# Optimization experiments

Hardware: AMD Instinct MI355X
Metric: run time of the kernel (lower is better)

The kernel has to match this reference:

```python
import jax, jax.numpy as jnp
import numpy as np

B, T, D, H = 2, 2048, 1024, 16
DH = D // H  # 64


def setup_inputs() -> dict:
    key = jax.random.key(0)
    ks = jax.random.split(key, 8)
    s = 0.02
    return {
        "x": jax.random.normal(ks[0], (B, T, D), jnp.float32),
        "mask": jnp.tril(jnp.ones((T, T), dtype=bool)),  # causal self-attention mask
        "wq": jax.random.normal(ks[1], (H, DH, D), jnp.float32) * s,
        "wk": jax.random.normal(ks[2], (H, DH, D), jnp.float32) * s,
        "wv": jax.random.normal(ks[3], (H, DH, D), jnp.float32) * s,
        "w1": jax.random.normal(ks[4], (4 * D, D), jnp.float32) * s,
        "b1": jnp.zeros((4 * D,), jnp.float32),
        "w2": jax.random.normal(ks[5], (D, 4 * D), jnp.float32) * s,
        "b2": jnp.zeros((D,), jnp.float32),
    }


def reference(x, mask, wq, wk, wv, w1, b1, w2, b2):
    # Per-head projections (MultiHeadLinear, bias=False, stacked on axis=-3):
    # q/k/v: [B, H, T, DH]
    q = jnp.einsum('btd,hed->bhte', x, wq)
    k = jnp.einsum('btd,hed->bhte', x, wk)
    v = jnp.einsum('btd,hed->bhte', x, wv)
    # logits = q @ k^T scaled by 1/sqrt(d_head): [B, H, T, T]
    logits = jnp.einsum('bhte,bhse->bhts', q, k) * (DH ** -0.5)
    logits = jnp.where(mask, logits, -jnp.inf)
    attn = jax.nn.softmax(logits, axis=-1)
    attn_out = jnp.einsum('bhts,bhse->bhte', attn, v)  # [B, H, T, DH]
    attn_out = jnp.transpose(attn_out, (0, 2, 1, 3)).reshape(B, T, D)
    # Note: output is x + ffw(x + attn_out) per the original forward.
    h = x + attn_out
    ffn = jax.nn.gelu(h @ w1.T + b1, approximate=False) @ w2.T + b2
    return x + ffn
```

## Files before the change

kernel.cpp:

```cpp
#include <hip/hip_runtime.h>
#include <hip/hip_bf16.h>
#include <cmath>

typedef __bf16 bf16;
typedef __bf16 bf16x8 __attribute__((ext_vector_type(8)));
typedef __bf16 bf16x4 __attribute__((ext_vector_type(4)));
typedef __bf16 bf16x2 __attribute__((ext_vector_type(2)));
typedef float  f32x4  __attribute__((ext_vector_type(4)));
typedef float  f32x16 __attribute__((ext_vector_type(16)));
typedef int    i32x4  __attribute__((ext_vector_type(4)));

#define B_   2
#define T_   2048
#define D_   1024
#define H_   16
#define DH_  64
#define BT_  (B_ * T_)
#define DFF_ (4 * D_)

#define GLDS(gp, lp) __builtin_amdgcn_global_load_lds( \
    (const __attribute__((address_space(1))) void*)(gp), \
    (__attribute__((address_space(3))) void*)(lp), 16, 0, 0)
#define VMCNT(n) asm volatile("s_waitcnt vmcnt(" #n ")" ::: "memory")

__global__ void cvt_f32_bf16(const float* __restrict__ src, bf16* __restrict__ dst, int n) {
    int i = (blockIdx.x * blockDim.x + threadIdx.x) * 4;
    if (i >= n) return;
    float4 v = *(const float4*)(src + i);
    bf16x4 o;
    o[0] = (bf16)v.x; o[1] = (bf16)v.y; o[2] = (bf16)v.z; o[3] = (bf16)v.w;
    *(bf16x4*)(dst + i) = o;
}

__device__ __forceinline__ float gelu_f(float v) {
    return 0.5f * v * (1.0f + erff(v * 0.70710678118654752f));
}

__device__ __forceinline__ int pkbf(float a, float b) {
    bf16x2 v; v[0] = (bf16)a; v[1] = (bf16)b;
    return __builtin_bit_cast(int, v);
}

__global__ __launch_bounds__(256) void transpose_v(
    const bf16* __restrict__ vrow, bf16* __restrict__ vt)
{
    __shared__ bf16 tile[64][72];
    const int tb = blockIdx.x;
    const int eb = blockIdx.y;
    const int b  = blockIdx.z;
    const int c  = threadIdx.x;

    const bf16* src = vrow + ((long)b * T_ + tb * 64) * 1024 + eb * 64;
    #pragma unroll
    for (int j = 0; j < 2; j++) {
        int ch = c + j * 256;
        int r = ch >> 3, s = ch & 7;
        *(bf16x8*)&tile[r][s * 8] = *(const bf16x8*)&src[(long)r * 1024 + s * 8];
    }
    __syncthreads();
    bf16* dst = vt + ((long)b * 1024 + eb * 64) * 2048 + tb * 64;
    #pragma unroll
    for (int j = 0; j < 2; j++) {
        int ch = c + j * 256;
        int r = ch >> 3, s = ch & 7;
        bf16x8 o;
        #pragma unroll
        for (int k = 0; k < 8; k++) o[k] = tile[s * 8 + k][r];
        *(bf16x8*)&dst[(long)r * 2048 + s * 8] = o;
    }
}

template <int EPI>
__global__ __launch_bounds__(256) void gemm_bt(
    const bf16* __restrict__ A, const bf16* __restrict__ Bt,
    void* __restrict__ outp, void* __restrict__ outp2, const float* __restrict__ bias,
    const float* __restrict__ resid, int M, int N, int K)
{
    __shared__ __align__(16) bf16 As[2][128 * 32];
    __shared__ __align__(16) bf16 Bs[2][128 * 32];
    const int tid  = threadIdx.x;
    const int lane = tid & 63;
    const int w    = tid >> 6;
    const int wr   = w >> 1, wc = w & 1;
    const int g    = lane >> 4, cc = lane & 15;
    const int m0   = blockIdx.y * 128, n0 = blockIdx.x * 128;
    const int NT   = K >> 5;

    f32x4 acc[4][4] = {};

    const int c0 = tid, c1 = tid + 256;
    const bf16* gA0 = A  + (long)(m0 + (c0 >> 2)) * K + ((c0 & 3) << 3);
    const bf16* gA1 = A  + (long)(m0 + (c1 >> 2)) * K + ((c1 & 3) << 3);
    const bf16* gB0 = Bt + (long)(n0 + (c0 >> 2)) * K + ((c0 & 3) << 3);
    const bf16* gB1 = Bt + (long)(n0 + (c1 >> 2)) * K + ((c1 & 3) << 3);

    auto stage = [&](int t) {
        const int buf = t & 1;
        const long k0 = (long)t << 5;
        GLDS(gA0 + k0, &As[buf][c0 * 8]);
        GLDS(gA1 + k0, &As[buf][c1 * 8]);
        GLDS(gB0 + k0, &Bs[buf][c0 * 8]);
        GLDS(gB1 + k0, &Bs[buf][c1 * 8]);
    };

    stage(0);
    VMCNT(0);
    __builtin_amdgcn_s_barrier();

    for (int t = 0; t < NT; ++t) {
        const bf16* Ab = As[t & 1];
        const bf16* Bb = Bs[t & 1];
        if (t + 1 < NT) stage(t + 1);

        bf16x8 af[4], bfr[4];
        #pragma unroll
        for (int mi = 0; mi < 4; mi++)
            af[mi] = *(const bf16x8*)&Ab[(wr * 64 + mi * 16 + cc) * 32 + g * 8];
        #pragma unroll
        for (int ni = 0; ni < 4; ni++)
            bfr[ni] = *(const bf16x8*)&Bb[(wc * 64 + ni * 16 + cc) * 32 + g * 8];
        #pragma unroll
        for (int mi = 0; mi < 4; mi++)
            #pragma unroll
            for (int ni = 0; ni < 4; ni++)
                acc[mi][ni] = __builtin_amdgcn_mfma_f32_16x16x32_bf16(af[mi], bfr[ni], acc[mi][ni], 0, 0, 0);

        VMCNT(0);
        __builtin_amdgcn_s_barrier();
    }

    #pragma unroll
    for (int mi = 0; mi < 4; mi++) {
        #pragma unroll
        for (int ni = 0; ni < 4; ni++) {
            #pragma unroll
            for (int r = 0; r < 4; r++) {
                int grow = m0 + wr * 64 + mi * 16 + g * 4 + r;
                int gcol = n0 + wc * 64 + ni * 16 + cc;
                float v = acc[mi][ni][r];
                if constexpr (EPI == 3) {
                    if (gcol < 2048)
                        ((bf16*)outp)[(long)grow * 2048 + gcol] = (bf16)v;
                    else
                        ((bf16*)outp2)[(long)grow * 1024 + (gcol - 2048)] = (bf16)v;
                } else if constexpr (EPI == 1) {
                    v += bias[gcol];
                    ((bf16*)outp)[(long)grow * N + gcol] = (bf16)gelu_f(v);
                } else {
                    v += bias[gcol] + resid[(long)grow * N + gcol];
                    ((float*)outp)[(long)grow * N + gcol] = v;
                }
            }
        }
    }
}

__global__ __launch_bounds__(256) void attn_kernel(
    const bf16* __restrict__ qk, const bf16* __restrict__ vt,
    const float* __restrict__ x, bf16* __restrict__ hout)
{
    __shared__ __align__(16) bf16 Ks[2][64 * 64];
    __shared__ __align__(16) bf16 Vs[2][64 * 64];
    const int tid  = threadIdx.x;
    const int lane = tid & 63, w = tid >> 6;
    const int l31 = lane & 31, hi = lane >> 5;
    const int qb = gridDim.x - 1 - blockIdx.x;
    const int hh = blockIdx.y, b = blockIdx.z;
    const int qbase = qb * 128;
    const int qw0 = qbase + w * 32;
    const int qg  = qw0 + l31;

    const bf16* qkb   = qk + (long)b * T_ * 2048;
    const bf16* kbase = qkb + 1024 + hh * 64;
    const bf16* vbase = vt + ((long)b * 1024 + hh * 64) * 2048;

    bf16x8 qf[4];
    {
        const bf16* qrow = qkb + (long)qg * 2048 + hh * 64;
        #pragma unroll
        for (int ks = 0; ks < 4; ks++) {
            bf16x8 v = *(const bf16x8*)&qrow[ks * 16 + hi * 8];
            #pragma unroll
            for (int j = 0; j < 8; j++) v[j] = (bf16)((float)v[j] * 0.125f);
            qf[ks] = v;
        }
    }

    float m_run = -INFINITY, l_run = 0.f;
    f32x16 o0 = {}, o1 = {};

    const int ntiles = (qbase >> 6) + 2;
    const int my_end = ((qw0 + 31) >> 6) + 1;

    auto stage = [&](int i) {
        const int buf = i & 1;
        const long kv0 = (long)i << 6;
        #pragma unroll
        for (int j = 0; j < 2; j++) {
            int c = tid + j * 256;
            int r = c >> 3, s = c & 7;
            int seg = (s ^ (r & 7)) << 3;
            GLDS(kbase + (kv0 + r) * 2048 + seg, &Ks[buf][c * 8]);
            GLDS(vbase + (long)r * 2048 + kv0 + seg, &Vs[buf][c * 8]);
        }
    };

    stage(0);
    __syncthreads();

    for (int i = 0; i < ntiles; ++i) {
        const int buf = i & 1;
        const int kv0 = i << 6;
        if (i + 1 < ntiles) stage(i + 1);

        if (i < my_end) {
            f32x16 s0 = {}, s1 = {};
            const int xk = l31 & 7;
            #pragma unroll
            for (int ks = 0; ks < 4; ks++) {
                int slot = ((2 * ks + hi) ^ xk) << 3;
                bf16x8 kf0 = *(const bf16x8*)&Ks[buf][l31 * 64 + slot];
                bf16x8 kf1 = *(const bf16x8*)&Ks[buf][(32 + l31) * 64 + slot];
                s0 = __builtin_amdgcn_mfma_f32_32x32x16_bf16(kf0, qf[ks], s0, 0, 0, 0);
                s1 = __builtin_amdgcn_mfma_f32_32x32x16_bf16(kf1, qf[ks], s1, 0, 0, 0);
            }

            if (kv0 + 64 > qw0) {
                #pragma unroll
                for (int r = 0; r < 16; r++) {
                    int kvr = kv0 + (r & 3) + 8 * (r >> 2) + 4 * hi;
                    if (kvr > qg)      s0[r] = -INFINITY;
                    if (kvr + 32 > qg) s1[r] = -INFINITY;
                }
            }

            float pm = s0[0];
            #pragma unroll
            for (int r = 1; r < 16; r++) pm = fmaxf(pm, s0[r]);
            #pragma unroll
            for (int r = 0; r < 16; r++) pm = fmaxf(pm, s1[r]);
            pm = fmaxf(pm, __shfl_xor(pm, 32));

            if (!__all(pm <= m_run + 8.f)) {
                float mn = fmaxf(m_run, pm);
                float al = __expf(m_run - mn);
                m_run = mn;
                l_run *= al;
                #pragma unroll
                for (int r = 0; r < 16; r++) {
                    float av = __shfl(al, (r & 3) + 8 * (r >> 2) + 4 * hi);
                    o0[r] *= av; o1[r] *= av;
                }
            }

            float rs = 0.f;
            #pragma unroll
            for (int r = 0; r < 16; r++) { float p = __expf(s0[r] - m_run); s0[r] = p; rs += p; }
            #pragma unroll
            for (int r = 0; r < 16; r++) { float p = __expf(s1[r] - m_run); s1[r] = p; rs += p; }
            rs += __shfl_xor(rs, 32);
            l_run += rs;

            i32x4 pw[4];
            {
                int d0[4], d1[4];
                #pragma unroll
                for (int m = 0; m < 4; m++) {
                    d0[m] = pkbf(s0[4 * m],     s0[4 * m + 1]);
                    d1[m] = pkbf(s0[4 * m + 2], s0[4 * m + 3]);
                }
                #pragma unroll
                for (int k2 = 0; k2 < 2; k2++) {
                    int r0 = __shfl_xor(d0[2 * k2 + 1 - hi], 32);
                    int r1 = __shfl_xor(d1[2 * k2 + 1 - hi], 32);
                    i32x4 t;
                    t[0] = hi ? r0 : d0[2 * k2];
                    t[1] = hi ? r1 : d1[2 * k2];
                    t[2] = hi ? d0[2 * k2 + 1] : r0;
                    t[3] = hi ? d1[2 * k2 + 1] : r1;
                    pw[k2] = t;
                }
            }
            {
                int d0[4], d1[4];
                #pragma unroll
                for (int m = 0; m < 4; m++) {
                    d0[m] = pkbf(s1[4 * m],     s1[4 * m + 1]);
                    d1[m] = pkbf(s1[4 * m + 2], s1[4 * m + 3]);
                }
                #pragma unroll
                for (int k2 = 0; k2 < 2; k2++) {
                    int r0 = __shfl_xor(d0[2 * k2 + 1 - hi], 32);
                    int r1 = __shfl_xor(d1[2 * k2 + 1 - hi], 32);
                    i32x4 t;
                    t[0] = hi ? r0 : d0[2 * k2];
                    t[1] = hi ? r1 : d1[2 * k2];
                    t[2] = hi ? d0[2 * k2 + 1] : r0;
                    t[3] = hi ? d1[2 * k2 + 1] : r1;
                    pw[2 + k2] = t;
                }
            }

            #pragma unroll
            for (int sl = 0; sl < 4; sl++) {
                bf16x8 pa = __builtin_bit_cast(bf16x8, pw[sl]);
                int slot = ((2 * sl + hi) ^ xk) << 3;
                bf16x8 vf0 = *(const bf16x8*)&Vs[buf][l31 * 64 + slot];
                bf16x8 vf1 = *(const bf16x8*)&Vs[buf][(32 + l31) * 64 + slot];
                o0 = __builtin_amdgcn_mfma_f32_32x32x16_bf16(pa, vf0, o0, 0, 0, 0);
                o1 = __builtin_amdgcn_mfma_f32_32x32x16_bf16(pa, vf1, o1, 0, 0, 0);
            }
        }
        __syncthreads();
    }

    #pragma unroll
    for (int r = 0; r < 16; r++) {
        int qr = (r & 3) + 8 * (r >> 2) + 4 * hi;
        float lr = __shfl(l_run, qr);
        int grow = qbase + w * 32 + qr;
        long base = ((long)b * T_ + grow) * 1024 + hh * 64 + l31;
        hout[base]      = (bf16)(x[base]      + o0[r] / lr);
        hout[base + 32] = (bf16)(x[base + 32] + o1[r] / lr);
    }
}

extern "C" void kernel_launch(void* const* d_in, const int* in_sizes, int n_in,
                              void* d_out, int out_size, void* d_ws, size_t ws_size,
                              hipStream_t stream) {
    const float* x  = (const float*)d_in[0];
    const float* wq = (const float*)d_in[2];
    const float* wk = (const float*)d_in[3];
    const float* wv = (const float*)d_in[4];
    const float* w1 = (const float*)d_in[5];
    const float* b1 = (const float*)d_in[6];
    const float* w2 = (const float*)d_in[7];
    const float* b2 = (const float*)d_in[8];
    float* out = (float*)d_out;

    char* ws = (char*)d_ws;
    bf16* xb   = (bf16*)(ws);
    bf16* wall = (bf16*)(ws + (8L  << 20));
    bf16* w1b  = (bf16*)(ws + (14L << 20));
    bf16* w2b  = (bf16*)(ws + (22L << 20));
    bf16* qkb  = (bf16*)(ws + (30L << 20));
    bf16* vtb  = (bf16*)(ws + (46L << 20));
    bf16* hbuf = (bf16*)(ws + (54L << 20));
    bf16* abuf = (bf16*)(ws + (62L << 20));
    bf16* vrow = hbuf;

    auto cvt = [&](const float* s, bf16* d, int n) {
        cvt_f32_bf16<<<(n / 4 + 255) / 256, 256, 0, stream>>>(s, d, n);
    };
    cvt(x,  xb,              BT_ * D_);
    cvt(wq, wall,            D_ * D_);
    cvt(wk, wall + D_ * D_,  D_ * D_);
    cvt(wv, wall + 2 * D_ * D_, D_ * D_);
    cvt(w1, w1b, DFF_ * D_);
    cvt(w2, w2b, D_ * DFF_);

    gemm_bt<3><<<dim3(3 * D_ / 128, BT_ / 128), 256, 0, stream>>>(
        xb, wall, qkb, vrow, nullptr, nullptr, BT_, 3 * D_, D_);

    transpose_v<<<dim3(T_ / 64, D_ / 64, B_), 256, 0, stream>>>(vrow, vtb);

    attn_kernel<<<dim3(T_ / 128, H_, B_), 256, 0, stream>>>(qkb, vtb, x, hbuf);

    gemm_bt<1><<<dim3(DFF_ / 128, BT_ / 128), 256, 0, stream>>>(
        hbuf, w1b, abuf, nullptr, b1, nullptr, BT_, DFF_, D_);

    gemm_bt<2><<<dim3(D_ / 128, BT_ / 128), 256, 0, stream>>>(
        abuf, w2b, out, nullptr, b2, x, BT_, D_, DFF_);
}
```

Baseline: 275.2 us.

## Load GEMM B operand directly to registers and swizzle A LDS layout

The B tile in the bf16 GEMM is no longer staged through LDS. Each wave now loads its B fragments straight from global memory into registers, double-buffered by unrolling the K loop by two. The A tile keeps its LDS path but gets an XOR swizzle on the 16-byte chunk index to reduce bank conflicts on fragment reads. This halves LDS traffic and footprint, which may help occupancy. The cost is redundant global loads of B across the two wave rows, since both wr waves fetch the same B, plus more registers. The unroll assumes an even number of K tiles.

Measured after the change: 359.5 us. 30.6% more time.

```diff
diff --git a/kernel.cpp b/kernel.cpp
--- a/kernel.cpp
+++ b/kernel.cpp
@@ -77,7 +77,6 @@
     const float* __restrict__ resid, int M, int N, int K)
 {
     __shared__ __align__(16) bf16 As[2][128 * 32];
-    __shared__ __align__(16) bf16 Bs[2][128 * 32];
     const int tid  = threadIdx.x;
     const int lane = tid & 63;
     const int w    = tid >> 6;
@@ -85,46 +84,60 @@
     const int g    = lane >> 4, cc = lane & 15;
     const int m0   = blockIdx.y * 128, n0 = blockIdx.x * 128;
     const int NT   = K >> 5;
+    const int akey = (cc >> 1) & 3;
 
     f32x4 acc[4][4] = {};
 
     const int c0 = tid, c1 = tid + 256;
-    const bf16* gA0 = A  + (long)(m0 + (c0 >> 2)) * K + ((c0 & 3) << 3);
-    const bf16* gA1 = A  + (long)(m0 + (c1 >> 2)) * K + ((c1 & 3) << 3);
-    const bf16* gB0 = Bt + (long)(n0 + (c0 >> 2)) * K + ((c0 & 3) << 3);
-    const bf16* gB1 = Bt + (long)(n0 + (c1 >> 2)) * K + ((c1 & 3) << 3);
-
-    auto stage = [&](int t) {
+    const int r0 = c0 >> 2, s0 = (((c0 & 3) ^ ((r0 >> 1) & 3)) << 3);
+    const int r1 = c1 >> 2, s1 = (((c1 & 3) ^ ((r1 >> 1) & 3)) << 3);
+    const bf16* gA0 = A + (long)(m0 + r0) * K + s0;
+    const bf16* gA1 = A + (long)(m0 + r1) * K + s1;
+
+    auto stageA = [&](int t) {
         const int buf = t & 1;
         const long k0 = (long)t << 5;
         GLDS(gA0 + k0, &As[buf][c0 * 8]);
         GLDS(gA1 + k0, &As[buf][c1 * 8]);
-        GLDS(gB0 + k0, &Bs[buf][c0 * 8]);
-        GLDS(gB1 + k0, &Bs[buf][c1 * 8]);
-    };
-
-    stage(0);
+    };
+
+    const bf16* gBr = Bt + (long)(n0 + wc * 64 + cc) * K + g * 8;
+    bf16x8 bqA[4], bqB[4];
+    auto loadB_A = [&](int t) {
+        #pragma unroll
+        for (int ni = 0; ni < 4; ni++)
+            bqA[ni] = *(const bf16x8*)(gBr + (long)ni * 16 * K + ((long)t << 5));
+    };
+    auto loadB_B = [&](int t) {
+        #pragma unroll
+        for (int ni = 0; ni < 4; ni++)
+            bqB[ni] = *(const bf16x8*)(gBr + (long)ni * 16 * K + ((long)t << 5));
+    };
+
+    auto compute = [&](const bf16* Ab, const bf16x8* bq) {
+        bf16x8 af[4];
+        #pragma unroll
+        for (int mi = 0; mi < 4; mi++)
+            af[mi] = *(const bf16x8*)&Ab[(wr * 64 + mi * 16 + cc) * 32 + ((g ^ akey) << 3)];
+        #pragma unroll
+        for (int mi = 0; mi < 4; mi++)
+            #pragma unroll
+            for (int ni = 0; ni < 4; ni++)
+                acc[mi][ni] = __builtin_amdgcn_mfma_f32_16x16x32_bf16(af[mi], bq[ni], acc[mi][ni], 0, 0, 0);
+    };
+
+    stageA(0);
+    loadB_A(0);
     VMCNT(0);
     __builtin_amdgcn_s_barrier();
 
-    for (int t = 0; t < NT; ++t) {
-        const bf16* Ab = As[t & 1];
-        const bf16* Bb = Bs[t & 1];
-        if (t + 1 < NT) stage(t + 1);
-
-        bf16x8 af[4], bfr[4];
-        #pragma unroll
-        for (int mi = 0; mi < 4; mi++)
-            af[mi] = *(const bf16x8*)&Ab[(wr * 64 + mi * 16 + cc) * 32 + g * 8];
-        #pragma unroll
-        for (int ni = 0; ni < 4; ni++)
-            bfr[ni] = *(const bf16x8*)&Bb[(wc * 64 + ni * 16 + cc) * 32 + g * 8];
-        #pragma unroll
-        for (int mi = 0; mi < 4; mi++)
-            #pragma unroll
-            for (int ni = 0; ni < 4; ni++)
-                acc[mi][ni] = __builtin_amdgcn_mfma_f32_16x16x32_bf16(af[mi], bfr[ni], acc[mi][ni], 0, 0, 0);
-
+    for (int t = 0; t < NT; t += 2) {
+        if (t + 1 < NT) { stageA(t + 1); loadB_B(t + 1); }
+        compute(As[0], bqA);
+        VMCNT(0);
+        __builtin_amdgcn_s_barrier();
+        if (t + 2 < NT) { stageA(t + 2); loadB_A(t + 2); }
+        compute(As[1], bqB);
         VMCNT(0);
         __builtin_amdgcn_s_barrier();
     }
```
